# Optimization experiments

Hardware: AMD Instinct MI355X
Metric: run time of the kernel (lower is better)

Reference implementation:

```python
import jax, jax.numpy as jnp
import numpy as np

FEAT = 64      # feature_dim
HEADS = 4      # n_head
LATENT = 256   # latent_dim
G = 128        # num graphs
NPG = 150      # nodes per graph (<=180 for one-hot positions)
N = G * NPG    # 19200 nodes
E = N * 12     # 230400 edges (excl. self loops)
POS = 180      # one-hot position classes
SLOPE = 0.2    # PyG GATConv leaky_relu negative slope


def gat_conv(x, src, dst, W, att_s, att_d, bias):
    """PyG GATConv (concat heads, self loops already appended to src/dst)."""
    n = x.shape[0]
    h = (x @ W).reshape(n, HEADS, FEAT)                 # [N,H,F]
    a_s = jnp.sum(h * att_s, axis=-1)                   # [N,H]
    a_d = jnp.sum(h * att_d, axis=-1)                   # [N,H]
    e = jax.nn.leaky_relu(a_s[src] + a_d[dst], SLOPE)   # [E,H] per-edge logits
    m = jax.ops.segment_max(e, dst, num_segments=n)     # segment softmax over dst
    ex = jnp.exp(e - m[dst])
    s = jax.ops.segment_sum(ex, dst, num_segments=n)
    alpha = ex / (s[dst] + 1e-16)
    out = jax.ops.segment_sum(h[src] * alpha[:, :, None], dst, num_segments=n)
    return out.reshape(n, HEADS * FEAT) + bias


def setup_inputs() -> dict:
    key = jax.random.key(0)
    ks = jax.random.split(key, 20)

    def p(k, shape, fan_in):
        return jax.random.normal(k, shape, jnp.float32) / np.sqrt(fan_in).astype(np.float32)

    z = jax.random.normal(ks[0], (G, LATENT), jnp.float32)
    src = jax.random.randint(ks[1], (E,), 0, N, jnp.int32)
    dst = (src + jax.random.randint(ks[2], (E,), 1, N, jnp.int32)) % N  # no self loops
    edge_index = jnp.stack([src, dst])
    batch = jnp.repeat(jnp.arange(G, dtype=jnp.int32), NPG)

    in1 = FEAT + POS
    in2 = FEAT * HEADS
    inp = dict(z=z, edge_index=edge_index, batch=batch, num_graphs=G)
    inp.update(
        W0=p(ks[3], (LATENT, FEAT), LATENT), b0=jnp.zeros(FEAT, jnp.float32),
        W1=p(ks[4], (in1, HEADS * FEAT), in1),
        as1=p(ks[5], (HEADS, FEAT), FEAT), ad1=p(ks[6], (HEADS, FEAT), FEAT),
        bb1=jnp.zeros(HEADS * FEAT, jnp.float32),
        W2=p(ks[7], (in2, HEADS * FEAT), in2),
        as2=p(ks[8], (HEADS, FEAT), FEAT), ad2=p(ks[9], (HEADS, FEAT), FEAT),
        bb2=jnp.zeros(HEADS * FEAT, jnp.float32),
        W3=p(ks[10], (in2, HEADS * FEAT), in2),
        as3=p(ks[11], (HEADS, FEAT), FEAT), ad3=p(ks[12], (HEADS, FEAT), FEAT),
        bb3=jnp.zeros(HEADS * FEAT, jnp.float32),
        Wg=p(ks[13], (in2, FEAT), in2), bg=jnp.zeros(FEAT, jnp.float32),
        Wf=p(ks[14], (FEAT, 5), FEAT), bf=jnp.zeros(5, jnp.float32),
    )
    return inp


def reference(z, edge_index, batch, num_graphs,
              W0, b0, W1, as1, ad1, bb1, W2, as2, ad2, bb2,
              W3, as3, ad3, bb3, Wg, bg, Wf, bf):
    n = batch.shape[0]
    x = z @ W0 + b0                                    # dec_feature_init
    x = x[batch]                                       # broadcast graph latent to nodes
    # node_order_within_batch (batch is sorted)
    counts = jax.ops.segment_sum(jnp.ones_like(batch), batch, num_segments=num_graphs)
    starts = jnp.cumsum(counts) - counts
    order = jnp.arange(n, dtype=batch.dtype) - starts[batch]
    pos = jax.nn.one_hot(order, POS, dtype=x.dtype)
    x = jax.nn.relu(jnp.concatenate([x, pos], axis=1))
    # GATConv adds self loops by default
    loops = jnp.arange(n, dtype=edge_index.dtype)
    src = jnp.concatenate([edge_index[0], loops])
    dst = jnp.concatenate([edge_index[1], loops])
    x = jax.nn.relu(gat_conv(x, src, dst, W1, as1, ad1, bb1))
    x = jax.nn.relu(gat_conv(x, src, dst, W2, as2, ad2, bb2))
    x = jax.nn.relu(gat_conv(x, src, dst, W3, as3, ad3, bb3))
    x = jax.nn.relu(x @ Wg + bg)                       # dec_geo
    return x @ Wf + bf                                 # fc_geo -> [N,5]
```

## Files before the change

### kernel.cpp

```cpp
#include <hip/hip_runtime.h>
#include <hip/hip_fp16.h>

#define GNUM 128
#define HEADS 4
#define FEAT 64
#define CH 256
#define LAT 256
#define SLOPE 0.2f
#define CAP 64
#define POSMAX 180

typedef _Float16 h16;
typedef __attribute__((ext_vector_type(4))) _Float16 half4;
typedef __attribute__((ext_vector_type(8))) _Float16 half8;
typedef __attribute__((ext_vector_type(4))) float floatx4;

__device__ __forceinline__ float lrelu(float x) { return fmaxf(x, SLOPE * x); }

__global__ __launch_bounds__(256) void k_setup(const int* __restrict__ batch, int* __restrict__ cnt,
                                               int* __restrict__ starts, int n,
                                               const float* __restrict__ W2, const float* __restrict__ W3,
                                               const float* __restrict__ Wg, h16* __restrict__ W2T,
                                               h16* __restrict__ W3T, h16* __restrict__ WgT,
                                               const float* __restrict__ z, const float* __restrict__ W0,
                                               const float* __restrict__ b0, const float* __restrict__ W1,
                                               const float* __restrict__ as1, const float* __restrict__ ad1,
                                               float* __restrict__ A, float* __restrict__ asg,
                                               float* __restrict__ adg, float* __restrict__ asp,
                                               float* __restrict__ adp) {
  __shared__ float red[4][FEAT];
  __shared__ float xzs[FEAT];
  int bx = blockIdx.x, t = threadIdx.x;
  if (bx < 576) {
    int idx = bx * 256 + t;
    if (idx < n) {
      cnt[idx] = 0;
      int b = batch[idx];
      if (idx == 0 || batch[idx - 1] != b) starts[b] = idx;
    }
    if (idx < 65536) {
      int kb = idx >> 13, rem = idx & 8191, j = rem >> 8, nn = rem & 255;
      W2T[kb * 8192 + nn * 32 + j] = (h16)W2[(kb * 32 + j) * 256 + nn];
    } else if (idx < 131072) {
      int l = idx - 65536;
      int kb = l >> 13, rem = l & 8191, j = rem >> 8, nn = rem & 255;
      W3T[kb * 8192 + nn * 32 + j] = (h16)W3[(kb * 32 + j) * 256 + nn];
    } else {
      int l = idx - 131072;
      int kb = l >> 11, rem = l & 2047, j = rem >> 6, nn = rem & 63;
      WgT[kb * 2048 + nn * 32 + j] = (h16)Wg[(kb * 32 + j) * 64 + nn];
    }
  } else if (bx < 576 + GNUM) {
    int g = bx - 576;
    int f = t & 63, kq = t >> 6;
    float acc = 0.f;
    for (int k = kq * 64; k < kq * 64 + 64; ++k) acc += z[g * LAT + k] * W0[k * FEAT + f];
    red[kq][f] = acc;
    __syncthreads();
    if (kq == 0)
      xzs[f] = fmaxf(red[0][f] + red[1][f] + red[2][f] + red[3][f] + b0[f], 0.f);
    __syncthreads();
    float a2 = 0.f;
#pragma unroll 16
    for (int k = 0; k < FEAT; ++k) a2 += xzs[k] * W1[k * CH + t];
    A[g * CH + t] = a2;
    float ps = a2 * as1[t], pd = a2 * ad1[t];
#pragma unroll
    for (int sh = 1; sh < 64; sh <<= 1) {
      ps += __shfl_xor(ps, sh, 64);
      pd += __shfl_xor(pd, sh, 64);
    }
    if ((t & 63) == 0) {
      asg[g * 4 + (t >> 6)] = ps;
      adg[g * 4 + (t >> 6)] = pd;
    }
  } else {
    int p = bx - (576 + GNUM);
    float wv = W1[(size_t)(FEAT + p) * CH + t];
    float ps = wv * as1[t], pd = wv * ad1[t];
#pragma unroll
    for (int sh = 1; sh < 64; sh <<= 1) {
      ps += __shfl_xor(ps, sh, 64);
      pd += __shfl_xor(pd, sh, 64);
    }
    if ((t & 63) == 0) {
      asp[p * 4 + (t >> 6)] = ps;
      adp[p * 4 + (t >> 6)] = pd;
    }
  }
}

__global__ __launch_bounds__(256) void k_H1(const float* __restrict__ A, const float* __restrict__ W1,
                                            const int* __restrict__ batch, const int* __restrict__ starts,
                                            const float* __restrict__ asg, const float* __restrict__ adg,
                                            const float* __restrict__ asp, const float* __restrict__ adp,
                                            h16* __restrict__ H16, float* __restrict__ a_s,
                                            float* __restrict__ a_d, int n) {
  int t = threadIdx.x;
  int row = blockIdx.x * 8 + (t >> 5);
  if (row < n) {
    int g = batch[row];
    int p = row - starts[g];
    int c0 = (t & 31) * 8;
    const float* ap = A + g * CH + c0;
    const float* wp = W1 + (size_t)(FEAT + p) * CH + c0;
    float4 a0 = *(const float4*)ap;
    float4 a1 = *(const float4*)(ap + 4);
    float4 w0v = *(const float4*)wp;
    float4 w1v = *(const float4*)(wp + 4);
    half8 o;
    o[0] = (h16)(a0.x + w0v.x); o[1] = (h16)(a0.y + w0v.y);
    o[2] = (h16)(a0.z + w0v.z); o[3] = (h16)(a0.w + w0v.w);
    o[4] = (h16)(a1.x + w1v.x); o[5] = (h16)(a1.y + w1v.y);
    o[6] = (h16)(a1.z + w1v.z); o[7] = (h16)(a1.w + w1v.w);
    *(half8*)(H16 + (size_t)row * CH + c0) = o;
  }
  int idx = blockIdx.x * 256 + t;
  if (idx < n * 4) {
    int nn = idx >> 2, h = idx & 3;
    int g2 = batch[nn], p2 = nn - starts[g2];
    a_s[idx] = asg[g2 * 4 + h] + asp[p2 * 4 + h];
    a_d[idx] = adg[g2 * 4 + h] + adp[p2 * 4 + h];
  }
}

__global__ void k_scatter(const int* __restrict__ src, const int* __restrict__ dst,
                          int* __restrict__ cnt, int* __restrict__ bucket, int e) {
  int i = blockIdx.x * blockDim.x + threadIdx.x;
  if (i < e) {
    int d = dst[i];
    int p = atomicAdd(&cnt[d], 1);
    if (p < CAP) bucket[d * CAP + p] = src[i];
  }
}

__global__ __launch_bounds__(256) void k_galpha(const h16* __restrict__ H16, const float* __restrict__ a_s,
                                                const float* __restrict__ a_d, const float* __restrict__ bias,
                                                const int* __restrict__ cnt, const int* __restrict__ bucket,
                                                h16* __restrict__ X16) {
  __shared__ float wsh[4][CAP][4];
  __shared__ int bsh[4][CAP];
  int wv = threadIdx.x >> 6, lane = threadIdx.x & 63;
  int n = blockIdx.x * 4 + wv;
  int c = min(cnt[n], CAP);
  bool valid = lane < c;
  int sc = valid ? bucket[n * CAP + lane] : n;
  if (valid) bsh[wv][lane] = sc;
  float4 ea4 = *(const float4*)(a_s + (size_t)sc * 4);
  float4 sn4 = *(const float4*)(a_s + (size_t)n * 4);
  float4 dn4 = *(const float4*)(a_d + (size_t)n * 4);
  float ea[4] = {ea4.x, ea4.y, ea4.z, ea4.w};
  float sn[4] = {sn4.x, sn4.y, sn4.z, sn4.w};
  float dn[4] = {dn4.x, dn4.y, dn4.z, dn4.w};
  float asf[4];
#pragma unroll
  for (int h = 0; h < 4; ++h) {
    float e = valid ? lrelu(ea[h] + dn[h]) : -1e30f;
    float es = lrelu(sn[h] + dn[h]);
    float m = e;
#pragma unroll
    for (int sh = 1; sh < 64; sh <<= 1) m = fmaxf(m, __shfl_xor(m, sh, 64));
    m = fmaxf(m, es);
    float wgt = valid ? __expf(e - m) : 0.f;
    float ws = __expf(es - m);
    float s = wgt;
#pragma unroll
    for (int sh = 1; sh < 64; sh <<= 1) s += __shfl_xor(s, sh, 64);
    s += ws;
    float inv = 1.f / (s + 1e-16f);
    if (valid) wsh[wv][lane][h] = wgt * inv;
    asf[h] = ws * inv;
  }
  __syncthreads();
  int hh = lane >> 4;
  int fo = lane * 4;
  half4 hv = *(const half4*)(H16 + (size_t)n * CH + fo);
  float a_self = asf[hh];
  float acc0 = a_self * (float)hv[0];
  float acc1 = a_self * (float)hv[1];
  float acc2 = a_self * (float)hv[2];
  float acc3 = a_self * (float)hv[3];
  if (c > 0) {
    int s2 = bsh[wv][0];
    half4 hs = *(const half4*)(H16 + (size_t)s2 * CH + fo);
    for (int j = 0; j < c; ++j) {
      float wj = wsh[wv][j][hh];
      half4 hc = hs;
      if (j + 1 < c) {
        int s3 = bsh[wv][j + 1];
        hs = *(const half4*)(H16 + (size_t)s3 * CH + fo);
      }
      acc0 += wj * (float)hc[0];
      acc1 += wj * (float)hc[1];
      acc2 += wj * (float)hc[2];
      acc3 += wj * (float)hc[3];
    }
  }
  float4 b4 = *(const float4*)(bias + fo);
  half4 o;
  o[0] = (h16)fmaxf(acc0 + b4.x, 0.f);
  o[1] = (h16)fmaxf(acc1 + b4.y, 0.f);
  o[2] = (h16)fmaxf(acc2 + b4.z, 0.f);
  o[3] = (h16)fmaxf(acc3 + b4.w, 0.f);
  *(half4*)(X16 + (size_t)n * CH + fo) = o;
}

__global__ __launch_bounds__(256) void k_gemm(const h16* __restrict__ X16, const h16* __restrict__ WT,
                                              const float* __restrict__ att_s, const float* __restrict__ att_d,
                                              h16* __restrict__ H16, float* __restrict__ a_s,
                                              float* __restrict__ a_d) {
  __shared__ __align__(16) char smem[80 * 264 * 2];
  h16* As = (h16*)smem;
  h16* Bs = (h16*)(smem + 6400);
  h16* Ht = (h16*)smem;
  int t = threadIdx.x;
  int w = t >> 6, lane = t & 63;
  int quad = lane >> 4, l15 = lane & 15;
  int row0 = blockIdx.x * 80;
  int arow = t >> 2, aseg = t & 3;
  floatx4 acc[5][4];
#pragma unroll
  for (int i = 0; i < 5; ++i)
#pragma unroll
    for (int j = 0; j < 4; ++j) acc[i][j] = (floatx4){0.f, 0.f, 0.f, 0.f};
  half8 ra0, ra1, rb0, rb1, rb2, rb3;
  ra0 = *(const half8*)(X16 + (size_t)(row0 + arow) * CH + aseg * 8);
  if (t < 64) ra1 = *(const half8*)(X16 + (size_t)(row0 + arow + 64) * CH + aseg * 8);
  {
    const h16* s = WT + t * 32;
    rb0 = *(const half8*)(s + 0);  rb1 = *(const half8*)(s + 8);
    rb2 = *(const half8*)(s + 16); rb3 = *(const half8*)(s + 24);
  }
  for (int kb = 0; kb < 8; ++kb) {
    __syncthreads();
    *(half8*)&As[arow * 40 + aseg * 8] = ra0;
    if (t < 64) *(half8*)&As[(arow + 64) * 40 + aseg * 8] = ra1;
    {
      h16* bd = &Bs[t * 40];
      *(half8*)(bd + 0) = rb0;  *(half8*)(bd + 8) = rb1;
      *(half8*)(bd + 16) = rb2; *(half8*)(bd + 24) = rb3;
    }
    __syncthreads();
    if (kb < 7) {
      ra0 = *(const half8*)(X16 + (size_t)(row0 + arow) * CH + (kb + 1) * 32 + aseg * 8);
      if (t < 64)
        ra1 = *(const half8*)(X16 + (size_t)(row0 + arow + 64) * CH + (kb + 1) * 32 + aseg * 8);
      const h16* s = WT + (kb + 1) * 8192 + t * 32;
      rb0 = *(const half8*)(s + 0);  rb1 = *(const half8*)(s + 8);
      rb2 = *(const half8*)(s + 16); rb3 = *(const half8*)(s + 24);
    }
    half8 af[5], bf[4];
#pragma unroll
    for (int mt = 0; mt < 5; ++mt) af[mt] = *(const half8*)&As[(mt * 16 + l15) * 40 + quad * 8];
#pragma unroll
    for (int nt = 0; nt < 4; ++nt)
      bf[nt] = *(const half8*)&Bs[(w * 64 + nt * 16 + l15) * 40 + quad * 8];
#pragma unroll
    for (int mt = 0; mt < 5; ++mt)
#pragma unroll
      for (int nt = 0; nt < 4; ++nt)
        acc[mt][nt] = __builtin_amdgcn_mfma_f32_16x16x32_f16(af[mt], bf[nt], acc[mt][nt], 0, 0, 0);
  }
  __syncthreads();
#pragma unroll
  for (int mt = 0; mt < 5; ++mt)
#pragma unroll
    for (int nt = 0; nt < 4; ++nt)
#pragma unroll
      for (int r = 0; r < 4; ++r)
        Ht[(mt * 16 + quad * 4 + r) * 264 + w * 64 + nt * 16 + l15] = (h16)acc[mt][nt][r];
  float asv[4], adv[4];
#pragma unroll
  for (int nt = 0; nt < 4; ++nt) {
    asv[nt] = att_s[w * FEAT + nt * 16 + l15];
    adv[nt] = att_d[w * FEAT + nt * 16 + l15];
  }
#pragma unroll
  for (int mt = 0; mt < 5; ++mt)
#pragma unroll
    for (int r = 0; r < 4; ++r) {
      float ps = acc[mt][0][r] * asv[0] + acc[mt][1][r] * asv[1] +
                 acc[mt][2][r] * asv[2] + acc[mt][3][r] * asv[3];
      float pd = acc[mt][0][r] * adv[0] + acc[mt][1][r] * adv[1] +
                 acc[mt][2][r] * adv[2] + acc[mt][3][r] * adv[3];
#pragma unroll
      for (int sh = 1; sh < 16; sh <<= 1) {
        ps += __shfl_xor(ps, sh, 16);
        pd += __shfl_xor(pd, sh, 16);
      }
      if (l15 == 0) {
        int row = row0 + mt * 16 + quad * 4 + r;
        a_s[row * 4 + w] = ps;
        a_d[row * 4 + w] = pd;
      }
    }
  __syncthreads();
  for (int rr = t >> 2; rr < 80; rr += 64) {
    const h16* srcr = &Ht[rr * 264 + aseg * 64];
    h16* dstr = H16 + (size_t)(row0 + rr) * CH + aseg * 64;
#pragma unroll
    for (int i = 0; i < 8; ++i) *(half8*)(dstr + i * 8) = *(const half8*)(srcr + i * 8);
  }
}

__global__ __launch_bounds__(256) void k_head(const h16* __restrict__ X16, const h16* __restrict__ WgT,
                                              const float* __restrict__ bg, const float* __restrict__ Wf,
                                              const float* __restrict__ bfv, float* __restrict__ out) {
  __shared__ __align__(16) char smem[80 * 68 * 4];
  h16* As = (h16*)smem;
  h16* Bs = (h16*)(smem + 6400);
  float* ytile = (float*)smem;
  __shared__ float WfS[FEAT * 5];
  int t = threadIdx.x;
  int w = t >> 6, lane = t & 63;
  int quad = lane >> 4, l15 = lane & 15;
  int row0 = blockIdx.x * 80;
  int arow = t >> 2, aseg = t & 3;
  for (int i = t; i < FEAT * 5; i += 256) WfS[i] = Wf[i];
  floatx4 acc[5];
#pragma unroll
  for (int mt = 0; mt < 5; ++mt) acc[mt] = (floatx4){0.f, 0.f, 0.f, 0.f};
  half8 ra0, ra1, rb;
  ra0 = *(const half8*)(X16 + (size_t)(row0 + arow) * CH + aseg * 8);
  if (t < 64) ra1 = *(const half8*)(X16 + (size_t)(row0 + arow + 64) * CH + aseg * 8);
  rb = *(const half8*)(WgT + arow * 32 + aseg * 8);
  for (int kb = 0; kb < 8; ++kb) {
    __syncthreads();
    *(half8*)&As[arow * 40 + aseg * 8] = ra0;
    if (t < 64) *(half8*)&As[(arow + 64) * 40 + aseg * 8] = ra1;
    *(half8*)&Bs[arow * 40 + aseg * 8] = rb;
    __syncthreads();
    if (kb < 7) {
      ra0 = *(const half8*)(X16 + (size_t)(row0 + arow) * CH + (kb + 1) * 32 + aseg * 8);
      if (t < 64)
        ra1 = *(const half8*)(X16 + (size_t)(row0 + arow + 64) * CH + (kb + 1) * 32 + aseg * 8);
      rb = *(const half8*)(WgT + (kb + 1) * 2048 + arow * 32 + aseg * 8);
    }
    half8 af[5], bfr;
#pragma unroll
    for (int mt = 0; mt < 5; ++mt) af[mt] = *(const half8*)&As[(mt * 16 + l15) * 40 + quad * 8];
    bfr = *(const half8*)&Bs[(w * 16 + l15) * 40 + quad * 8];
#pragma unroll
    for (int mt = 0; mt < 5; ++mt)
      acc[mt] = __builtin_amdgcn_mfma_f32_16x16x32_f16(af[mt], bfr, acc[mt], 0, 0, 0);
  }
  __syncthreads();
  int col = w * 16 + l15;
  float bgv = bg[col];
#pragma unroll
  for (int mt = 0; mt < 5; ++mt)
#pragma unroll
    for (int r = 0; r < 4; ++r)
      ytile[(mt * 16 + quad * 4 + r) * 68 + col] = fmaxf(acc[mt][r] + bgv, 0.f);
  __syncthreads();
  for (int i = t; i < 80 * 5; i += 256) {
    int row = i / 5, o = i % 5;
    float s = bfv[o];
#pragma unroll
    for (int k = 0; k < FEAT; ++k) s += ytile[row * 68 + k] * WfS[k * 5 + o];
    out[(size_t)(row0 + row) * 5 + o] = s;
  }
}

static inline size_t alignup(size_t x) { return (x + 255) & ~(size_t)255; }

extern "C" void kernel_launch(void* const* d_in, const int* in_sizes, int n_in,
                              void* d_out, int out_size, void* d_ws, size_t ws_size,
                              hipStream_t stream) {
  (void)n_in; (void)out_size; (void)ws_size;
  const float* z   = (const float*)d_in[0];
  const int* edge  = (const int*)d_in[1];
  const int* batch = (const int*)d_in[2];
  const float* W0  = (const float*)d_in[4];
  const float* b0  = (const float*)d_in[5];
  const float* W1  = (const float*)d_in[6];
  const float* as1 = (const float*)d_in[7];
  const float* ad1 = (const float*)d_in[8];
  const float* bb1 = (const float*)d_in[9];
  const float* W2  = (const float*)d_in[10];
  const float* as2 = (const float*)d_in[11];
  const float* ad2 = (const float*)d_in[12];
  const float* bb2 = (const float*)d_in[13];
  const float* W3  = (const float*)d_in[14];
  const float* as3 = (const float*)d_in[15];
  const float* ad3 = (const float*)d_in[16];
  const float* bb3 = (const float*)d_in[17];
  const float* Wg  = (const float*)d_in[18];
  const float* bg  = (const float*)d_in[19];
  const float* Wf  = (const float*)d_in[20];
  const float* bfv = (const float*)d_in[21];
  float* out = (float*)d_out;

  const int E = in_sizes[1] / 2;
  const int N = in_sizes[2];
  const int* srcI = edge;
  const int* dstI = edge + E;

  char* w = (char*)d_ws;
  auto carve = [&](size_t bytes) { void* p = (void*)w; w += alignup(bytes); return p; };
  int* starts  = (int*)carve((size_t)GNUM * 4);
  int* cnt     = (int*)carve((size_t)N * 4);
  int* bucket  = (int*)carve((size_t)N * CAP * 4);
  float* A     = (float*)carve((size_t)GNUM * CH * 4);
  float* a_s   = (float*)carve((size_t)N * 4 * 4);
  float* a_d   = (float*)carve((size_t)N * 4 * 4);
  float* asg   = (float*)carve((size_t)GNUM * 4 * 4);
  float* adg   = (float*)carve((size_t)GNUM * 4 * 4);
  float* asp   = (float*)carve((size_t)POSMAX * 4 * 4);
  float* adp   = (float*)carve((size_t)POSMAX * 4 * 4);
  h16* W2T     = (h16*)carve((size_t)CH * CH * 2);
  h16* W3T     = (h16*)carve((size_t)CH * CH * 2);
  h16* WgT     = (h16*)carve((size_t)CH * FEAT * 2);
  h16* H16     = (h16*)carve((size_t)N * CH * 2);
  h16* X16     = (h16*)carve((size_t)N * CH * 2);

  int eb256 = (E + 255) / 256;

  hipLaunchKernelGGL(k_setup, dim3(576 + GNUM + POSMAX), dim3(256), 0, stream,
                     batch, cnt, starts, N, W2, W3, Wg, W2T, W3T, WgT, z, W0, b0, W1,
                     as1, ad1, A, asg, adg, asp, adp);
  hipLaunchKernelGGL(k_H1, dim3(N / 8), dim3(256), 0, stream,
                     A, W1, batch, starts, asg, adg, asp, adp, H16, a_s, a_d, N);
  hipLaunchKernelGGL(k_scatter, dim3(eb256), dim3(256), 0, stream, srcI, dstI, cnt, bucket, E);

  hipLaunchKernelGGL(k_galpha, dim3(N / 4), dim3(256), 0, stream, H16, a_s, a_d, bb1, cnt, bucket, X16);
  hipLaunchKernelGGL(k_gemm, dim3(N / 80), dim3(256), 0, stream, X16, W2T, as2, ad2, H16, a_s, a_d);
  hipLaunchKernelGGL(k_galpha, dim3(N / 4), dim3(256), 0, stream, H16, a_s, a_d, bb2, cnt, bucket, X16);
  hipLaunchKernelGGL(k_gemm, dim3(N / 80), dim3(256), 0, stream, X16, W3T, as3, ad3, H16, a_s, a_d);
  hipLaunchKernelGGL(k_galpha, dim3(N / 4), dim3(256), 0, stream, H16, a_s, a_d, bb3, cnt, bucket, X16);
  hipLaunchKernelGGL(k_head, dim3(N / 80), dim3(256), 0, stream, X16, WgT, bg, Wf, bfv, out);
}
```

Measured before the change: 280.7 us.

## Fuse attention aggregation with following GEMM per 16-row tile, merge scatter

Merges the H1 construction and edge bucketing into one launch. Fuses each GAT aggregation with the next layer's weight GEMM, and the last aggregation with the head MLP, so aggregated features stay in shared memory instead of making a round trip through global memory. Adds ping-pong H/a_s/a_d buffers. In exchange, each 16-row block reloads the full weight matrix from global/L2 with no register prefetch, and the per-node loop adds extra barriers, which lowers GEMM efficiency.

Result: slower. 340.2 us (+21.2%).

```diff
diff --git a/kernel.cpp b/kernel.cpp
--- a/kernel.cpp
+++ b/kernel.cpp
@@ -90,271 +90,290 @@
   }
 }
 
-__global__ __launch_bounds__(256) void k_H1(const float* __restrict__ A, const float* __restrict__ W1,
-                                            const int* __restrict__ batch, const int* __restrict__ starts,
-                                            const float* __restrict__ asg, const float* __restrict__ adg,
-                                            const float* __restrict__ asp, const float* __restrict__ adp,
-                                            h16* __restrict__ H16, float* __restrict__ a_s,
-                                            float* __restrict__ a_d, int n) {
+__global__ __launch_bounds__(256) void k_pre(const float* __restrict__ A, const float* __restrict__ W1,
+                                             const int* __restrict__ batch, const int* __restrict__ starts,
+                                             const float* __restrict__ asg, const float* __restrict__ adg,
+                                             const float* __restrict__ asp, const float* __restrict__ adp,
+                                             h16* __restrict__ H16, float* __restrict__ a_s,
+                                             float* __restrict__ a_d, int n,
+                                             const int* __restrict__ src, const int* __restrict__ dst,
+                                             int* __restrict__ cnt, int* __restrict__ bucket, int e,
+                                             int h1blocks) {
   int t = threadIdx.x;
-  int row = blockIdx.x * 8 + (t >> 5);
-  if (row < n) {
-    int g = batch[row];
-    int p = row - starts[g];
-    int c0 = (t & 31) * 8;
-    const float* ap = A + g * CH + c0;
-    const float* wp = W1 + (size_t)(FEAT + p) * CH + c0;
-    float4 a0 = *(const float4*)ap;
-    float4 a1 = *(const float4*)(ap + 4);
-    float4 w0v = *(const float4*)wp;
-    float4 w1v = *(const float4*)(wp + 4);
-    half8 o;
-    o[0] = (h16)(a0.x + w0v.x); o[1] = (h16)(a0.y + w0v.y);
-    o[2] = (h16)(a0.z + w0v.z); o[3] = (h16)(a0.w + w0v.w);
-    o[4] = (h16)(a1.x + w1v.x); o[5] = (h16)(a1.y + w1v.y);
-    o[6] = (h16)(a1.z + w1v.z); o[7] = (h16)(a1.w + w1v.w);
-    *(half8*)(H16 + (size_t)row * CH + c0) = o;
-  }
-  int idx = blockIdx.x * 256 + t;
-  if (idx < n * 4) {
-    int nn = idx >> 2, h = idx & 3;
-    int g2 = batch[nn], p2 = nn - starts[g2];
-    a_s[idx] = asg[g2 * 4 + h] + asp[p2 * 4 + h];
-    a_d[idx] = adg[g2 * 4 + h] + adp[p2 * 4 + h];
+  if ((int)blockIdx.x < h1blocks) {
+    int row = blockIdx.x * 8 + (t >> 5);
+    if (row < n) {
+      int g = batch[row];
+      int p = row - starts[g];
+      int c0 = (t & 31) * 8;
+      const float* ap = A + g * CH + c0;
+      const float* wp = W1 + (size_t)(FEAT + p) * CH + c0;
+      float4 a0 = *(const float4*)ap;
+      float4 a1 = *(const float4*)(ap + 4);
+      float4 w0v = *(const float4*)wp;
+      float4 w1v = *(const float4*)(wp + 4);
+      half8 o;
+      o[0] = (h16)(a0.x + w0v.x); o[1] = (h16)(a0.y + w0v.y);
+      o[2] = (h16)(a0.z + w0v.z); o[3] = (h16)(a0.w + w0v.w);
+      o[4] = (h16)(a1.x + w1v.x); o[5] = (h16)(a1.y + w1v.y);
+      o[6] = (h16)(a1.z + w1v.z); o[7] = (h16)(a1.w + w1v.w);
+      *(half8*)(H16 + (size_t)row * CH + c0) = o;
+    }
+    int idx = blockIdx.x * 256 + t;
+    if (idx < n * 4) {
+      int nn = idx >> 2, h = idx & 3;
+      int g2 = batch[nn], p2 = nn - starts[g2];
+      a_s[idx] = asg[g2 * 4 + h] + asp[p2 * 4 + h];
+      a_d[idx] = adg[g2 * 4 + h] + adp[p2 * 4 + h];
+    }
+  } else {
+    int i = (blockIdx.x - h1blocks) * 256 + t;
+    if (i < e) {
+      int d = dst[i];
+      int p = atomicAdd(&cnt[d], 1);
+      if (p < CAP) bucket[d * CAP + p] = src[i];
+    }
   }
 }
 
-__global__ void k_scatter(const int* __restrict__ src, const int* __restrict__ dst,
-                          int* __restrict__ cnt, int* __restrict__ bucket, int e) {
-  int i = blockIdx.x * blockDim.x + threadIdx.x;
-  if (i < e) {
-    int d = dst[i];
-    int p = atomicAdd(&cnt[d], 1);
-    if (p < CAP) bucket[d * CAP + p] = src[i];
-  }
-}
-
-__global__ __launch_bounds__(256) void k_galpha(const h16* __restrict__ H16, const float* __restrict__ a_s,
-                                                const float* __restrict__ a_d, const float* __restrict__ bias,
-                                                const int* __restrict__ cnt, const int* __restrict__ bucket,
-                                                h16* __restrict__ X16) {
+__global__ __launch_bounds__(256) void k_layer(const h16* __restrict__ H16i, const float* __restrict__ a_si,
+                                               const float* __restrict__ a_di, const float* __restrict__ bias,
+                                               const int* __restrict__ cnt, const int* __restrict__ bucket,
+                                               const h16* __restrict__ WT, const float* __restrict__ att_s,
+                                               const float* __restrict__ att_d, h16* __restrict__ H16o,
+                                               float* __restrict__ a_so, float* __restrict__ a_do_) {
+  __shared__ __align__(16) h16 Xs[16 * 264];
+  __shared__ __align__(16) h16 Bs[256 * 40];
   __shared__ float wsh[4][CAP][4];
   __shared__ int bsh[4][CAP];
-  int wv = threadIdx.x >> 6, lane = threadIdx.x & 63;
-  int n = blockIdx.x * 4 + wv;
-  int c = min(cnt[n], CAP);
-  bool valid = lane < c;
-  int sc = valid ? bucket[n * CAP + lane] : n;
-  if (valid) bsh[wv][lane] = sc;
-  float4 ea4 = *(const float4*)(a_s + (size_t)sc * 4);
-  float4 sn4 = *(const float4*)(a_s + (size_t)n * 4);
-  float4 dn4 = *(const float4*)(a_d + (size_t)n * 4);
-  float ea[4] = {ea4.x, ea4.y, ea4.z, ea4.w};
-  float sn[4] = {sn4.x, sn4.y, sn4.z, sn4.w};
-  float dn[4] = {dn4.x, dn4.y, dn4.z, dn4.w};
-  float asf[4];
-#pragma unroll
-  for (int h = 0; h < 4; ++h) {
-    float e = valid ? lrelu(ea[h] + dn[h]) : -1e30f;
-    float es = lrelu(sn[h] + dn[h]);
-    float m = e;
-#pragma unroll
-    for (int sh = 1; sh < 64; sh <<= 1) m = fmaxf(m, __shfl_xor(m, sh, 64));
-    m = fmaxf(m, es);
-    float wgt = valid ? __expf(e - m) : 0.f;
-    float ws = __expf(es - m);
-    float s = wgt;
-#pragma unroll
-    for (int sh = 1; sh < 64; sh <<= 1) s += __shfl_xor(s, sh, 64);
-    s += ws;
-    float inv = 1.f / (s + 1e-16f);
-    if (valid) wsh[wv][lane][h] = wgt * inv;
-    asf[h] = ws * inv;
+  int t = threadIdx.x, wv = t >> 6, lane = t & 63;
+  int quad = lane >> 4, l15 = lane & 15;
+  int row0 = blockIdx.x * 16;
+  int hh = lane >> 4, fo = lane * 4;
+  for (int i = 0; i < 4; ++i) {
+    int n = row0 + wv * 4 + i;
+    int c = min(cnt[n], CAP);
+    bool valid = lane < c;
+    int sc = valid ? bucket[n * CAP + lane] : n;
+    if (valid) bsh[wv][lane] = sc;
+    float4 ea4 = *(const float4*)(a_si + (size_t)sc * 4);
+    float4 sn4 = *(const float4*)(a_si + (size_t)n * 4);
+    float4 dn4 = *(const float4*)(a_di + (size_t)n * 4);
+    float ea[4] = {ea4.x, ea4.y, ea4.z, ea4.w};
+    float sn[4] = {sn4.x, sn4.y, sn4.z, sn4.w};
+    float dn[4] = {dn4.x, dn4.y, dn4.z, dn4.w};
+    float asf[4];
+#pragma unroll
+    for (int h = 0; h < 4; ++h) {
+      float e = valid ? lrelu(ea[h] + dn[h]) : -1e30f;
+      float es = lrelu(sn[h] + dn[h]);
+      float m = e;
+#pragma unroll
+      for (int sh = 1; sh < 64; sh <<= 1) m = fmaxf(m, __shfl_xor(m, sh, 64));
+      m = fmaxf(m, es);
+      float wgt = valid ? __expf(e - m) : 0.f;
+      float ws = __expf(es - m);
+      float s = wgt;
+#pragma unroll
+      for (int sh = 1; sh < 64; sh <<= 1) s += __shfl_xor(s, sh, 64);
+      s += ws;
+      float inv = 1.f / (s + 1e-16f);
+      if (valid) wsh[wv][lane][h] = wgt * inv;
+      asf[h] = ws * inv;
+    }
+    __syncthreads();
+    half4 hv = *(const half4*)(H16i + (size_t)n * CH + fo);
+    float a_self = asf[hh];
+    float acc0 = a_self * (float)hv[0];
+    float acc1 = a_self * (float)hv[1];
+    float acc2 = a_self * (float)hv[2];
+    float acc3 = a_self * (float)hv[3];
+    if (c > 0) {
+      int s2 = bsh[wv][0];
+      half4 hs = *(const half4*)(H16i + (size_t)s2 * CH + fo);
+      for (int j = 0; j < c; ++j) {
+        float wj = wsh[wv][j][hh];
+        half4 hc = hs;
+        if (j + 1 < c) {
+          int s3 = bsh[wv][j + 1];
+          hs = *(const half4*)(H16i + (size_t)s3 * CH + fo);
+        }
+        acc0 += wj * (float)hc[0];
+        acc1 += wj * (float)hc[1];
+        acc2 += wj * (float)hc[2];
+        acc3 += wj * (float)hc[3];
+      }
+    }
+    float4 b4 = *(const float4*)(bias + fo);
+    half4 o;
+    o[0] = (h16)fmaxf(acc0 + b4.x, 0.f);
+    o[1] = (h16)fmaxf(acc1 + b4.y, 0.f);
+    o[2] = (h16)fmaxf(acc2 + b4.z, 0.f);
+    o[3] = (h16)fmaxf(acc3 + b4.w, 0.f);
+    *(half4*)&Xs[(wv * 4 + i) * 264 + fo] = o;
+    __syncthreads();
+  }
+  floatx4 acc[4];
+#pragma unroll
+  for (int nt = 0; nt < 4; ++nt) acc[nt] = (floatx4){0.f, 0.f, 0.f, 0.f};
+  for (int kb = 0; kb < 8; ++kb) {
+    if (kb) __syncthreads();
+    {
+      const h16* s = WT + kb * 8192 + t * 32;
+      h16* bd = &Bs[t * 40];
+      *(half8*)(bd + 0)  = *(const half8*)(s + 0);
+      *(half8*)(bd + 8)  = *(const half8*)(s + 8);
+      *(half8*)(bd + 16) = *(const half8*)(s + 16);
+      *(half8*)(bd + 24) = *(const half8*)(s + 24);
+    }
+    __syncthreads();
+    half8 af = *(const half8*)&Xs[l15 * 264 + kb * 32 + quad * 8];
+    half8 bf[4];
+#pragma unroll
+    for (int nt = 0; nt < 4; ++nt)
+      bf[nt] = *(const half8*)&Bs[(wv * 64 + nt * 16 + l15) * 40 + quad * 8];
+#pragma unroll
+    for (int nt = 0; nt < 4; ++nt)
+      acc[nt] = __builtin_amdgcn_mfma_f32_16x16x32_f16(af, bf[nt], acc[nt], 0, 0, 0);
   }
   __syncthreads();
-  int hh = lane >> 4;
-  int fo = lane * 4;
-  half4 hv = *(const half4*)(H16 + (size_t)n * CH + fo);
-  float a_self = asf[hh];
-  float acc0 = a_self * (float)hv[0];
-  float acc1 = a_self * (float)hv[1];
-  float acc2 = a_self * (float)hv[2];
-  float acc3 = a_self * (float)hv[3];
-  if (c > 0) {
-    int s2 = bsh[wv][0];
-    half4 hs = *(const half4*)(H16 + (size_t)s2 * CH + fo);
-    for (int j = 0; j < c; ++j) {
-      float wj = wsh[wv][j][hh];
-      half4 hc = hs;
-      if (j + 1 < c) {
-        int s3 = bsh[wv][j + 1];
-        hs = *(const half4*)(H16 + (size_t)s3 * CH + fo);
+#pragma unroll
+  for (int nt = 0; nt < 4; ++nt)
+#pragma unroll
+    for (int r = 0; r < 4; ++r)
+      Xs[(quad * 4 + r) * 264 + wv * 64 + nt * 16 + l15] = (h16)acc[nt][r];
+  float asv[4], adv[4];
+#pragma unroll
+  for (int nt = 0; nt < 4; ++nt) {
+    asv[nt] = att_s[wv * FEAT + nt * 16 + l15];
+    adv[nt] = att_d[wv * FEAT + nt * 16 + l15];
+  }
+#pragma unroll
+  for (int r = 0; r < 4; ++r) {
+    float ps = acc[0][r] * asv[0] + acc[1][r] * asv[1] +
+               acc[2][r] * asv[2] + acc[3][r] * asv[3];
+    float pd = acc[0][r] * adv[0] + acc[1][r] * adv[1] +
+               acc[2][r] * adv[2] + acc[3][r] * adv[3];
+#pragma unroll
+    for (int sh = 1; sh < 16; sh <<= 1) {
+      ps += __shfl_xor(ps, sh, 16);
+      pd += __shfl_xor(pd, sh, 16);
+    }
+    if (l15 == 0) {
+      int row = row0 + quad * 4 + r;
+      a_so[row * 4 + wv] = ps;
+      a_do_[row * 4 + wv] = pd;
+    }
+  }
+  __syncthreads();
+  {
+    int row = t >> 4, seg = t & 15;
+    const h16* srcr = &Xs[row * 264 + seg * 16];
+    h16* dstr = H16o + (size_t)(row0 + row) * CH + seg * 16;
+    *(half8*)(dstr + 0) = *(const half8*)(srcr + 0);
+    *(half8*)(dstr + 8) = *(const half8*)(srcr + 8);
+  }
+}
+
+__global__ __launch_bounds__(256) void k_last(const h16* __restrict__ H16i, const float* __restrict__ a_si,
+                                              const float* __restrict__ a_di, const float* __restrict__ bias,
+                                              const int* __restrict__ cnt, const int* __restrict__ bucket,
+                                              const h16* __restrict__ WgT, const float* __restrict__ bg,
+                                              const float* __restrict__ Wf, const float* __restrict__ bfv,
+                                              float* __restrict__ out) {
+  __shared__ __align__(16) h16 Xs[16 * 264];
+  __shared__ __align__(16) h16 Bs[64 * 40];
+  __shared__ float wsh[4][CAP][4];
+  __shared__ int bsh[4][CAP];
+  __shared__ float WfS[FEAT * 5];
+  int t = threadIdx.x, wv = t >> 6, lane = t & 63;
+  int quad = lane >> 4, l15 = lane & 15;
+  int row0 = blockIdx.x * 16;
+  int hh = lane >> 4, fo = lane * 4;
+  for (int i = t; i < FEAT * 5; i += 256) WfS[i] = Wf[i];
+  for (int i = 0; i < 4; ++i) {
+    int n = row0 + wv * 4 + i;
+    int c = min(cnt[n], CAP);
+    bool valid = lane < c;
+    int sc = valid ? bucket[n * CAP + lane] : n;
+    if (valid) bsh[wv][lane] = sc;
+    float4 ea4 = *(const float4*)(a_si + (size_t)sc * 4);
+    float4 sn4 = *(const float4*)(a_si + (size_t)n * 4);
+    float4 dn4 = *(const float4*)(a_di + (size_t)n * 4);
+    float ea[4] = {ea4.x, ea4.y, ea4.z, ea4.w};
+    float sn[4] = {sn4.x, sn4.y, sn4.z, sn4.w};
+    float dn[4] = {dn4.x, dn4.y, dn4.z, dn4.w};
+    float asf[4];
+#pragma unroll
+    for (int h = 0; h < 4; ++h) {
+      float e = valid ? lrelu(ea[h] + dn[h]) : -1e30f;
+      float es = lrelu(sn[h] + dn[h]);
+      float m = e;
+#pragma unroll
+      for (int sh = 1; sh < 64; sh <<= 1) m = fmaxf(m, __shfl_xor(m, sh, 64));
+      m = fmaxf(m, es);
+      float wgt = valid ? __expf(e - m) : 0.f;
+      float ws = __expf(es - m);
+      float s = wgt;
+#pragma unroll
+      for (int sh = 1; sh < 64; sh <<= 1) s += __shfl_xor(s, sh, 64);
+      s += ws;
+      float inv = 1.f / (s + 1e-16f);
+      if (valid) wsh[wv][lane][h] = wgt * inv;
+      asf[h] = ws * inv;
+    }
+    __syncthreads();
+    half4 hv = *(const half4*)(H16i + (size_t)n * CH + fo);
+    float a_self = asf[hh];
+    float acc0 = a_self * (float)hv[0];
+    float acc1 = a_self * (float)hv[1];
+    float acc2 = a_self * (float)hv[2];
+    float acc3 = a_self * (float)hv[3];
+    if (c > 0) {
+      int s2 = bsh[wv][0];
+      half4 hs = *(const half4*)(H16i + (size_t)s2 * CH + fo);
+      for (int j = 0; j < c; ++j) {
+        float wj = wsh[wv][j][hh];
+        half4 hc = hs;
+        if (j + 1 < c) {
+          int s3 = bsh[wv][j + 1];
+          hs = *(const half4*)(H16i + (size_t)s3 * CH + fo);
+        }
+        acc0 += wj * (float)hc[0];
+        acc1 += wj * (float)hc[1];
+        acc2 += wj * (float)hc[2];
+        acc3 += wj * (float)hc[3];
       }
-      acc0 += wj * (float)hc[0];
-      acc1 += wj * (float)hc[1];
-      acc2 += wj * (float)hc[2];
-      acc3 += wj * (float)hc[3];
-    }
-  }
-  float4 b4 = *(const float4*)(bias + fo);
-  half4 o;
-  o[0] = (h16)fmaxf(acc0 + b4.x, 0.f);
-  o[1] = (h16)fmaxf(acc1 + b4.y, 0.f);
-  o[2] = (h16)fmaxf(acc2 + b4.z, 0.f);
-  o[3] = (h16)fmaxf(acc3 + b4.w, 0.f);
-  *(half4*)(X16 + (size_t)n * CH + fo) = o;
-}
-
-__global__ __launch_bounds__(256) void k_gemm(const h16* __restrict__ X16, const h16* __restrict__ WT,
-                                              const float* __restrict__ att_s, const float* __restrict__ att_d,
-                                              h16* __restrict__ H16, float* __restrict__ a_s,
-                                              float* __restrict__ a_d) {
-  __shared__ __align__(16) char smem[80 * 264 * 2];
-  h16* As = (h16*)smem;
-  h16* Bs = (h16*)(smem + 6400);
-  h16* Ht = (h16*)smem;
-  int t = threadIdx.x;
-  int w = t >> 6, lane = t & 63;
-  int quad = lane >> 4, l15 = lane & 15;
-  int row0 = blockIdx.x * 80;
-  int arow = t >> 2, aseg = t & 3;
-  floatx4 acc[5][4];
-#pragma unroll
-  for (int i = 0; i < 5; ++i)
-#pragma unroll
-    for (int j = 0; j < 4; ++j) acc[i][j] = (floatx4){0.f, 0.f, 0.f, 0.f};
-  half8 ra0, ra1, rb0, rb1, rb2, rb3;
-  ra0 = *(const half8*)(X16 + (size_t)(row0 + arow) * CH + aseg * 8);
-  if (t < 64) ra1 = *(const half8*)(X16 + (size_t)(row0 + arow + 64) * CH + aseg * 8);
-  {
-    const h16* s = WT + t * 32;
-    rb0 = *(const half8*)(s + 0);  rb1 = *(const half8*)(s + 8);
-    rb2 = *(const half8*)(s + 16); rb3 = *(const half8*)(s + 24);
-  }
+    }
+    float4 b4 = *(const float4*)(bias + fo);
+    half4 o;
+    o[0] = (h16)fmaxf(acc0 + b4.x, 0.f);
+    o[1] = (h16)fmaxf(acc1 + b4.y, 0.f);
+    o[2] = (h16)fmaxf(acc2 + b4.z, 0.f);
+    o[3] = (h16)fmaxf(acc3 + b4.w, 0.f);
+    *(half4*)&Xs[(wv * 4 + i) * 264 + fo] = o;
+    __syncthreads();
+  }
+  floatx4 acc = (floatx4){0.f, 0.f, 0.f, 0.f};
+  int brow = t >> 2, bseg = t & 3;
   for (int kb = 0; kb < 8; ++kb) {
-    __syncthreads();
-    *(half8*)&As[arow * 40 + aseg * 8] = ra0;
-    if (t < 64) *(half8*)&As[(arow + 64) * 40 + aseg * 8] = ra1;
-    {
-      h16* bd = &Bs[t * 40];
-      *(half8*)(bd + 0) = rb0;  *(half8*)(bd + 8) = rb1;
-      *(half8*)(bd + 16) = rb2; *(half8*)(bd + 24) = rb3;
-    }
-    __syncthreads();
-    if (kb < 7) {
-      ra0 = *(const half8*)(X16 + (size_t)(row0 + arow) * CH + (kb + 1) * 32 + aseg * 8);
-      if (t < 64)
-        ra1 = *(const half8*)(X16 + (size_t)(row0 + arow + 64) * CH + (kb + 1) * 32 + aseg * 8);
-      const h16* s = WT + (kb + 1) * 8192 + t * 32;
-      rb0 = *(const half8*)(s + 0);  rb1 = *(const half8*)(s + 8);
-      rb2 = *(const half8*)(s + 16); rb3 = *(const half8*)(s + 24);
-    }
-    half8 af[5], bf[4];
-#pragma unroll
-    for (int mt = 0; mt < 5; ++mt) af[mt] = *(const half8*)&As[(mt * 16 + l15) * 40 + quad * 8];
-#pragma unroll
-    for (int nt = 0; nt < 4; ++nt)
-      bf[nt] = *(const half8*)&Bs[(w * 64 + nt * 16 + l15) * 40 + quad * 8];
-#pragma unroll
-    for (int mt = 0; mt < 5; ++mt)
-#pragma unroll
-      for (int nt = 0; nt < 4; ++nt)
-        acc[mt][nt] = __builtin_amdgcn_mfma_f32_16x16x32_f16(af[mt], bf[nt], acc[mt][nt], 0, 0, 0);
+    if (kb) __syncthreads();
+    *(half8*)&Bs[brow * 40 + bseg * 8] = *(const half8*)(WgT + kb * 2048 + brow * 32 + bseg * 8);
+    __syncthreads();
+    half8 af = *(const half8*)&Xs[l15 * 264 + kb * 32 + quad * 8];
+    half8 bf = *(const half8*)&Bs[(wv * 16 + l15) * 40 + quad * 8];
+    acc = __builtin_amdgcn_mfma_f32_16x16x32_f16(af, bf, acc, 0, 0, 0);
   }
   __syncthreads();
-#pragma unroll
-  for (int mt = 0; mt < 5; ++mt)
-#pragma unroll
-    for (int nt = 0; nt < 4; ++nt)
-#pragma unroll
-      for (int r = 0; r < 4; ++r)
-        Ht[(mt * 16 + quad * 4 + r) * 264 + w * 64 + nt * 16 + l15] = (h16)acc[mt][nt][r];
-  float asv[4], adv[4];
-#pragma unroll
-  for (int nt = 0; nt < 4; ++nt) {
-    asv[nt] = att_s[w * FEAT + nt * 16 + l15];
-    adv[nt] = att_d[w * FEAT + nt * 16 + l15];
-  }
-#pragma unroll
-  for (int mt = 0; mt < 5; ++mt)
-#pragma unroll
-    for (int r = 0; r < 4; ++r) {
-      float ps = acc[mt][0][r] * asv[0] + acc[mt][1][r] * asv[1] +
-                 acc[mt][2][r] * asv[2] + acc[mt][3][r] * asv[3];
-      float pd = acc[mt][0][r] * adv[0] + acc[mt][1][r] * adv[1] +
-                 acc[mt][2][r] * adv[2] + acc[mt][3][r] * adv[3];
-#pragma unroll
-      for (int sh = 1; sh < 16; sh <<= 1) {
-        ps += __shfl_xor(ps, sh, 16);
-        pd += __shfl_xor(pd, sh, 16);
-      }
-      if (l15 == 0) {
-        int row = row0 + mt * 16 + quad * 4 + r;
-        a_s[row * 4 + w] = ps;
-        a_d[row * 4 + w] = pd;
-      }
-    }
+  float* ytile = (float*)Xs;
+  int col = wv * 16 + l15;
+  float bgv = bg[col];
+#pragma unroll
+  for (int r = 0; r < 4; ++r)
+    ytile[(quad * 4 + r) * 68 + col] = fmaxf(acc[r] + bgv, 0.f);
   __syncthreads();
-  for (int rr = t >> 2; rr < 80; rr += 64) {
-    const h16* srcr = &Ht[rr * 264 + aseg * 64];
-    h16* dstr = H16 + (size_t)(row0 + rr) * CH + aseg * 64;
-#pragma unroll
-    for (int i = 0; i < 8; ++i) *(half8*)(dstr + i * 8) = *(const half8*)(srcr + i * 8);
-  }
-}
-
-__global__ __launch_bounds__(256) void k_head(const h16* __restrict__ X16, const h16* __restrict__ WgT,
-                                              const float* __restrict__ bg, const float* __restrict__ Wf,
-                                              const float* __restrict__ bfv, float* __restrict__ out) {
-  __shared__ __align__(16) char smem[80 * 68 * 4];
-  h16* As = (h16*)smem;
-  h16* Bs = (h16*)(smem + 6400);
-  float* ytile = (float*)smem;
-  __shared__ float WfS[FEAT * 5];
-  int t = threadIdx.x;
-  int w = t >> 6, lane = t & 63;
-  int quad = lane >> 4, l15 = lane & 15;
-  int row0 = blockIdx.x * 80;
-  int arow = t >> 2, aseg = t & 3;
-  for (int i = t; i < FEAT * 5; i += 256) WfS[i] = Wf[i];
-  floatx4 acc[5];
-#pragma unroll
-  for (int mt = 0; mt < 5; ++mt) acc[mt] = (floatx4){0.f, 0.f, 0.f, 0.f};
-  half8 ra0, ra1, rb;
-  ra0 = *(const half8*)(X16 + (size_t)(row0 + arow) * CH + aseg * 8);
-  if (t < 64) ra1 = *(const half8*)(X16 + (size_t)(row0 + arow + 64) * CH + aseg * 8);
-  rb = *(const half8*)(WgT + arow * 32 + aseg * 8);
-  for (int kb = 0; kb < 8; ++kb) {
-    __syncthreads();
-    *(half8*)&As[arow * 40 + aseg * 8] = ra0;
-    if (t < 64) *(half8*)&As[(arow + 64) * 40 + aseg * 8] = ra1;
-    *(half8*)&Bs[arow * 40 + aseg * 8] = rb;
-    __syncthreads();
-    if (kb < 7) {
-      ra0 = *(const half8*)(X16 + (size_t)(row0 + arow) * CH + (kb + 1) * 32 + aseg * 8);
-      if (t < 64)
-        ra1 = *(const half8*)(X16 + (size_t)(row0 + arow + 64) * CH + (kb + 1) * 32 + aseg * 8);
-      rb = *(const half8*)(WgT + (kb + 1) * 2048 + arow * 32 + aseg * 8);
-    }
-    half8 af[5], bfr;
-#pragma unroll
-    for (int mt = 0; mt < 5; ++mt) af[mt] = *(const half8*)&As[(mt * 16 + l15) * 40 + quad * 8];
-    bfr = *(const half8*)&Bs[(w * 16 + l15) * 40 + quad * 8];
-#pragma unroll
-    for (int mt = 0; mt < 5; ++mt)
-      acc[mt] = __builtin_amdgcn_mfma_f32_16x16x32_f16(af[mt], bfr, acc[mt], 0, 0, 0);
-  }
-  __syncthreads();
-  int col = w * 16 + l15;
-  float bgv = bg[col];
-#pragma unroll
-  for (int mt = 0; mt < 5; ++mt)
-#pragma unroll
-    for (int r = 0; r < 4; ++r)
-      ytile[(mt * 16 + quad * 4 + r) * 68 + col] = fmaxf(acc[mt][r] + bgv, 0.f);
-  __syncthreads();
-  for (int i = t; i < 80 * 5; i += 256) {
-    int row = i / 5, o = i % 5;
+  if (t < 16 * 5) {
+    int row = t / 5, o = t % 5;
     float s = bfv[o];
 #pragma unroll
     for (int k = 0; k < FEAT; ++k) s += ytile[row * 68 + k] * WfS[k * 5 + o];
@@ -402,8 +421,10 @@
   int* cnt     = (int*)carve((size_t)N * 4);
   int* bucket  = (int*)carve((size_t)N * CAP * 4);
   float* A     = (float*)carve((size_t)GNUM * CH * 4);
-  float* a_s   = (float*)carve((size_t)N * 4 * 4);
-  float* a_d   = (float*)carve((size_t)N * 4 * 4);
+  float* a_sA  = (float*)carve((size_t)N * 4 * 4);
+  float* a_dA  = (float*)carve((size_t)N * 4 * 4);
+  float* a_sB  = (float*)carve((size_t)N * 4 * 4);
+  float* a_dB  = (float*)carve((size_t)N * 4 * 4);
   float* asg   = (float*)carve((size_t)GNUM * 4 * 4);
   float* adg   = (float*)carve((size_t)GNUM * 4 * 4);
   float* asp   = (float*)carve((size_t)POSMAX * 4 * 4);
@@ -411,22 +432,22 @@
   h16* W2T     = (h16*)carve((size_t)CH * CH * 2);
   h16* W3T     = (h16*)carve((size_t)CH * CH * 2);
   h16* WgT     = (h16*)carve((size_t)CH * FEAT * 2);
-  h16* H16     = (h16*)carve((size_t)N * CH * 2);
-  h16* X16     = (h16*)carve((size_t)N * CH * 2);
-
-  int eb256 = (E + 255) / 256;
+  h16* H16a    = (h16*)carve((size_t)N * CH * 2);
+  h16* H16b    = (h16*)carve((size_t)N * CH * 2);
+
+  int h1blocks = N / 8;
+  int ebl = (E + 255) / 256;
 
   hipLaunchKernelGGL(k_setup, dim3(576 + GNUM + POSMAX), dim3(256), 0, stream,
                      batch, cnt, starts, N, W2, W3, Wg, W2T, W3T, WgT, z, W0, b0, W1,
                      as1, ad1, A, asg, adg, asp, adp);
-  hipLaunchKernelGGL(k_H1, dim3(N / 8), dim3(256), 0, stream,
-                     A, W1, batch, starts, asg, adg, asp, adp, H16, a_s, a_d, N);
-  hipLaunchKernelGGL(k_scatter, dim3(eb256), dim3(256), 0, stream, srcI, dstI, cnt, bucket, E);
-
-  hipLaunchKernelGGL(k_galpha, dim3(N / 4), dim3(256), 0, stream, H16, a_s, a_d, bb1, cnt, bucket, X16);
-  hipLaunchKernelGGL(k_gemm, dim3(N / 80), dim3(256), 0, stream, X16, W2T, as2, ad2, H16, a_s, a_d);
-  hipLaunchKernelGGL(k_galpha, dim3(N / 4), dim3(256), 0, stream, H16, a_s, a_d, bb2, cnt, bucket, X16);
-  hipLaunchKernelGGL(k_gemm, dim3(N / 80), dim3(256), 0, stream, X16, W3T, as3, ad3, H16, a_s, a_d);
-  hipLaunchKernelGGL(k_galpha, dim3(N / 4), dim3(256), 0, stream, H16, a_s, a_d, bb3, cnt, bucket, X16);
-  hipLaunchKernelGGL(k_head, dim3(N / 80), dim3(256), 0, stream, X16, WgT, bg, Wf, bfv, out);
+  hipLaunchKernelGGL(k_pre, dim3(h1blocks + ebl), dim3(256), 0, stream,
+                     A, W1, batch, starts, asg, adg, asp, adp, H16a, a_sA, a_dA, N,
+                     srcI, dstI, cnt, bucket, E, h1blocks);
+  hipLaunchKernelGGL(k_layer, dim3(N / 16), dim3(256), 0, stream,
+                     H16a, a_sA, a_dA, bb1, cnt, bucket, W2T, as2, ad2, H16b, a_sB, a_dB);
+  hipLaunchKernelGGL(k_layer, dim3(N / 16), dim3(256), 0, stream,
+                     H16b, a_sB, a_dB, bb2, cnt, bucket, W3T, as3, ad3, H16a, a_sA, a_dA);
+  hipLaunchKernelGGL(k_last, dim3(N / 16), dim3(256), 0, stream,
+                     H16a, a_sA, a_dA, bb3, cnt, bucket, WgT, bg, Wf, bfv, out);
 }
```
